# Optimization experiments

Hardware: AMD Instinct MI355X
Metric: run time of the kernel (lower is better)

## Reference

```python
import jax, jax.numpy as jnp
import numpy as np

NUM_TAPS = 4096
LOWCUT, HIGHCUT, FS = 30.0, 1024.0, 4096
B, C, T = 8, 4, 131072


def firwin_bandpass(num_taps, low, high, fs):
    # Replicates scipy.signal.firwin(numtaps, [low, high], pass_zero=False, fs=fs)
    nyq = fs / 2.0
    l, h = low / nyq, high / nyq
    m = np.arange(num_taps) - (num_taps - 1) / 2.0
    h_ideal = h * np.sinc(h * m) - l * np.sinc(l * m)  # ideal bandpass
    hk = h_ideal * np.hamming(num_taps)  # symmetric Hamming (scipy default)
    fc = (l + h) / 2.0  # scale frequency = band midpoint
    hk = hk / np.sum(hk * np.cos(np.pi * m * fc))
    return hk.astype(np.float32)


def _fir_conv(x, kernel):
    # Depthwise 'same' cross-correlation matching torch conv1d(padding='same').
    # x: [B, C, T], kernel: [K]
    Cc = x.shape[1]
    K = kernel.shape[0]
    left, right = (K - 1) // 2, K // 2  # torch 'same' asymmetric pad for even K
    w = jnp.broadcast_to(kernel[None, None, :], (Cc, 1, K))  # [C,1,K] depthwise
    return jax.lax.conv_general_dilated(
        x, w, window_strides=(1,), padding=[(left, right)],
        dimension_numbers=('NCH', 'OIH', 'NCH'), feature_group_count=Cc)


def setup_inputs() -> dict:
    key = jax.random.key(0)
    x = jax.random.normal(key, (B, C, T), dtype=jnp.float32)
    kernel = jnp.asarray(firwin_bandpass(NUM_TAPS, LOWCUT, HIGHCUT, FS))
    return {"x": x, "kernel": kernel}


def reference(x, kernel):
    pad = NUM_TAPS // 2
    xp = jnp.pad(x, ((0, 0), (0, 0), (pad, pad)), mode='reflect')
    y = _fir_conv(xp, kernel)
    # zero-phase: filter time-reversed signal, reverse back
    y = _fir_conv(y[..., ::-1], kernel)[..., ::-1]
    return y[..., pad:-pad]
```

## Files before the change

### kernel.cpp

```cpp
#include <hip/hip_runtime.h>


#define T_LEN   131072
#define XE_LEN  139776
#define XE_U4   (XE_LEN / 8)
#define NCHUNK  312
#define QSTEPS  288
#define QQ      72
#define SCH     8
#define NCH     9
#define CW      64

typedef float  f32x4  __attribute__((ext_vector_type(4)));
typedef __bf16 bf16x8 __attribute__((ext_vector_type(8)));

#define WS_KZ   0
#define WS_G    49152
#define WS_AHI  81920
#define WS_XE   401408
#define WS_END  9347072

__device__ __forceinline__ void gload_lds16(const uint4* g, uint4* lds) {
  __builtin_amdgcn_global_load_lds(
      (const __attribute__((address_space(1))) unsigned int*)g,
      (__attribute__((address_space(3))) unsigned int*)lds, 16, 0, 0);
}

__global__ void k_build_kz(const float* __restrict__ k, float* __restrict__ kz,
                           float* __restrict__ g) {
  int m = blockIdx.x * 256 + threadIdx.x;
  if (m < 12288) {
    int i = m - 4096;
    kz[m] = (i >= 0 && i < 4096) ? k[i] : 0.0f;
  }
  if (m < 8192) g[m] = 0.0f;
}

__global__ void k_autocorr(const float* __restrict__ k,
                           const float* __restrict__ kz,
                           float* __restrict__ g) {
  int s = blockIdx.x * 256 + threadIdx.x;
  int i0 = blockIdx.y * 256;
  const float* kk  = k + i0;
  const float* kzs = kz + (8191 - s) + i0;
  float a0 = 0.f, a1 = 0.f, a2 = 0.f, a3 = 0.f;
  #pragma unroll 4
  for (int i = 0; i < 256; i += 4) {
    float4 kv = *(const float4*)(kk + i);
    float4 zv;
    __builtin_memcpy(&zv, kzs + i, 16);
    a0 = fmaf(kv.x, zv.x, a0);
    a1 = fmaf(kv.y, zv.y, a1);
    a2 = fmaf(kv.z, zv.z, a2);
    a3 = fmaf(kv.w, zv.w, a3);
  }
  atomicAdd(&g[s], (a0 + a1) + (a2 + a3));
}

__global__ void k_build_afrag(const float* __restrict__ g,
                              __bf16* __restrict__ Ahi) {
  int P = blockIdx.x;
  int t = threadIdx.x;
  int l = t >> 2;
  int jj0 = (t & 3) * 2;
  int q = l >> 4, i = l & 15;
  int p = P - 24;
  #pragma unroll
  for (int u = 0; u < 2; ++u) {
    int jj = jj0 + u;
    int s = 32 * p + 8 * q + jj - i;
    float val = (s >= 0 && s <= 8190) ? g[s] : 0.0f;
    Ahi[P * 512 + l * 8 + jj] = (__bf16)val;
  }
}

__global__ void k_build_xe(const float* __restrict__ x, __bf16* __restrict__ xe) {
  int e0 = (blockIdx.x * 256 + threadIdx.x) * 8;
  int row = blockIdx.y;
  if (e0 >= XE_LEN) return;
  const float* xr = x + (size_t)row * T_LEN;
  int v0 = e0 - 4095;
  bf16x8 outv;
  if (v0 >= 0 && v0 <= T_LEN - 8) {
    float4 f0, f1;
    __builtin_memcpy(&f0, xr + v0, 16);
    __builtin_memcpy(&f1, xr + v0 + 4, 16);
    outv[0] = (__bf16)f0.x; outv[1] = (__bf16)f0.y;
    outv[2] = (__bf16)f0.z; outv[3] = (__bf16)f0.w;
    outv[4] = (__bf16)f1.x; outv[5] = (__bf16)f1.y;
    outv[6] = (__bf16)f1.z; outv[7] = (__bf16)f1.w;
  } else {
    #pragma unroll
    for (int u = 0; u < 8; ++u) {
      int v = v0 + u;
      float val = 0.0f;
      if (v >= -2048 && v < T_LEN + 2048) {
        int v2 = v < 0 ? -v : v;
        v2 = v2 >= T_LEN ? 2 * T_LEN - 2 - v2 : v2;
        val = xr[v2];
      }
      outv[u] = (__bf16)val;
    }
  }
  ((uint4*)(xe + (size_t)row * XE_LEN))[e0 >> 3] =
      __builtin_bit_cast(uint4, outv);
}

__global__ __launch_bounds__(256, 2) void k_fir_mfma(
    const uint4* __restrict__ xeu, const uint4* __restrict__ Ahi,
    float* __restrict__ out) {
  __shared__ uint4 sbB[4096];

  const int tid = threadIdx.x;
  const int w   = tid >> 6;
  const int l   = tid & 63;
  const int q   = l >> 4;
  const int n   = l & 15;
  const int t0  = blockIdx.x << 10;
  const int rbase = blockIdx.y << 3;
  const int Qbeg  = w * QQ;
  const int lofs  = q + 2 * n;

  const uint4* gbase = xeu + (size_t)rbase * XE_U4 + (t0 >> 3) + 4 * Qbeg + l;
  uint4* sw = sbB + (w << 10);

  f32x4 acc[8][4];
  #pragma unroll
  for (int r = 0; r < 8; ++r)
    #pragma unroll
    for (int m = 0; m < 4; ++m) acc[r][m] = (f32x4){0.f, 0.f, 0.f, 0.f};

  #pragma unroll
  for (int r = 0; r < 8; ++r)
    gload_lds16(gbase + (size_t)r * XE_U4, sw + (r << 6));
  asm volatile("s_waitcnt vmcnt(0)" ::: "memory");

  int buf = 0;
  for (int ch = 0; ch < NCH; ++ch) {
    if (ch + 1 < NCH) {
      uint4* dst = sw + ((buf ^ 1) << 9);
      const uint4* src = gbase + ((ch + 1) << 5);
      #pragma unroll
      for (int r = 0; r < 8; ++r)
        gload_lds16(src + (size_t)r * XE_U4, dst + (r << 6));
    }

    const uint4* bw = sw + (buf << 9) + lofs;
    #pragma unroll 2
    for (int Qr = 0; Qr < SCH; ++Qr) {
      const int Q = Qbeg + (ch << 3) + Qr;
      bf16x8 A[4];
      #pragma unroll
      for (int mt = 0; mt < 4; ++mt)
        A[mt] = __builtin_bit_cast(bf16x8, Ahi[(Q + 24 - 8 * mt) * 64 + l]);
      #pragma unroll
      for (int r = 0; r < 8; ++r) {
        bf16x8 B = __builtin_bit_cast(bf16x8, bw[(r << 6) + 4 * Qr]);
        #pragma unroll
        for (int mt = 0; mt < 4; ++mt)
          acc[r][mt] =
              __builtin_amdgcn_mfma_f32_16x16x32_bf16(A[mt], B, acc[r][mt], 0, 0, 0);
      }
    }

    if (ch + 1 < NCH) {
      asm volatile("s_waitcnt vmcnt(0)" ::: "memory");
      buf ^= 1;
    }
  }

  __syncthreads();
  float* C = (float*)sbB;
  const int co = (q << 2) + (n << 4);
  #pragma unroll
  for (int ph = 0; ph < 4; ++ph) {
    const int mt = (w + ph) & 3;
    float* cp = C + (mt << 8) + co;
    if (ph == 0) {
      #pragma unroll
      for (int r = 0; r < 8; ++r)
        *(f32x4*)(cp + (r << 10)) = acc[r][mt];
    } else {
      #pragma unroll
      for (int r = 0; r < 8; ++r) {
        f32x4 v = *(f32x4*)(cp + (r << 10));
        v += acc[r][mt];
        *(f32x4*)(cp + (r << 10)) = v;
      }
    }
    __syncthreads();
  }

  #pragma unroll
  for (int u = 0; u < 8; ++u) {
    f32x4 v = ((f32x4*)C)[tid + (u << 8)];
    *(f32x4*)(out + (size_t)(rbase + u) * T_LEN + t0 + (tid << 2)) = v;
  }
}

extern "C" void kernel_launch(void* const* d_in, const int* in_sizes, int n_in,
                              void* d_out, int out_size, void* d_ws, size_t ws_size,
                              hipStream_t stream) {
  const float* x = (const float*)d_in[0];
  const float* k = (const float*)d_in[1];
  float* out = (float*)d_out;
  char* ws = (char*)d_ws;
  if (ws_size < (size_t)WS_END) return;

  float*  kz  = (float*)(ws + WS_KZ);
  float*  g   = (float*)(ws + WS_G);
  __bf16* Ahi = (__bf16*)(ws + WS_AHI);
  __bf16* xe  = (__bf16*)(ws + WS_XE);

  k_build_kz<<<dim3(48), dim3(256), 0, stream>>>(k, kz, g);
  k_autocorr<<<dim3(32, 16), dim3(256), 0, stream>>>(k, kz, g);
  k_build_afrag<<<dim3(NCHUNK), dim3(256), 0, stream>>>(g, Ahi);
  k_build_xe<<<dim3((XE_LEN / 8 + 255) / 256, 32), dim3(256), 0, stream>>>(x, xe);
  k_fir_mfma<<<dim3(T_LEN / 1024, 4), dim3(256), 0, stream>>>(
      (const uint4*)xe, (const uint4*)Ahi, out);
}
```

Before: 169.0 us.

## Fuse kz build into xe kernel, software-pipeline A loads, remap blocks across XCDs

Folds the kz/g initialisation into the xe build kernel, which removes one launch. The FIR MFMA main loop is flattened into a ping-pong step macro, so the A fragments for the next step are prefetched while the current MFMAs run, B values are loaded into registers up front, and s_setprio raises priority around the MFMA burst. The 2D grid becomes 1D with a block-index remap that interleaves blocks across XCDs for better L2 locality. Costs are higher register pressure from the double-buffered A fragments and a larger, more complex unrolled loop.

```diff
diff --git a/kernel.cpp b/kernel.cpp
--- a/kernel.cpp
+++ b/kernel.cpp
@@ -5,11 +5,9 @@
 #define XE_LEN  139776
 #define XE_U4   (XE_LEN / 8)
 #define NCHUNK  312
-#define QSTEPS  288
 #define QQ      72
 #define SCH     8
 #define NCH     9
-#define CW      64
 
 typedef float  f32x4  __attribute__((ext_vector_type(4)));
 typedef __bf16 bf16x8 __attribute__((ext_vector_type(8)));
@@ -24,16 +22,6 @@
   __builtin_amdgcn_global_load_lds(
       (const __attribute__((address_space(1))) unsigned int*)g,
       (__attribute__((address_space(3))) unsigned int*)lds, 16, 0, 0);
-}
-
-__global__ void k_build_kz(const float* __restrict__ k, float* __restrict__ kz,
-                           float* __restrict__ g) {
-  int m = blockIdx.x * 256 + threadIdx.x;
-  if (m < 12288) {
-    int i = m - 4096;
-    kz[m] = (i >= 0 && i < 4096) ? k[i] : 0.0f;
-  }
-  if (m < 8192) g[m] = 0.0f;
 }
 
 __global__ void k_autocorr(const float* __restrict__ k,
@@ -74,7 +62,17 @@
   }
 }
 
-__global__ void k_build_xe(const float* __restrict__ x, __bf16* __restrict__ xe) {
+__global__ void k_build_xe(const float* __restrict__ x, __bf16* __restrict__ xe,
+                           const float* __restrict__ k, float* __restrict__ kz,
+                           float* __restrict__ g) {
+  if (blockIdx.y == 0) {
+    int m = blockIdx.x * 256 + threadIdx.x;
+    if (m < 12288) {
+      int i = m - 4096;
+      kz[m] = (i >= 0 && i < 4096) ? k[i] : 0.0f;
+    }
+    if (m < 8192) g[m] = 0.0f;
+  }
   int e0 = (blockIdx.x * 256 + threadIdx.x) * 8;
   int row = blockIdx.y;
   if (e0 >= XE_LEN) return;
@@ -106,6 +104,45 @@
       __builtin_bit_cast(uint4, outv);
 }
 
+#define FIR_STEP(ACUR, ANXT)                                               \
+  {                                                                        \
+    const int ch = Qi >> 3, Qr = Qi & 7;                                   \
+    if (Qr == 0) {                                                         \
+      if (ch > 0) {                                                        \
+        asm volatile("s_waitcnt vmcnt(0)" ::: "memory");                   \
+        buf ^= 1;                                                          \
+      }                                                                    \
+      if (ch < NCH - 1) {                                                  \
+        uint4* dst = sw + ((buf ^ 1) << 9);                                \
+        const uint4* src = gbase + ((ch + 1) << 5);                        \
+        _Pragma("unroll")                                                  \
+        for (int r = 0; r < 8; ++r)                                        \
+          gload_lds16(src + (size_t)r * XE_U4, dst + (r << 6));            \
+      }                                                                    \
+    }                                                                      \
+    const uint4* bp = sw + (buf << 9) + lofs + (Qr << 2);                  \
+    bf16x8 Bv[8];                                                          \
+    _Pragma("unroll")                                                      \
+    for (int r = 0; r < 8; ++r)                                            \
+      Bv[r] = __builtin_bit_cast(bf16x8, bp[r << 6]);                      \
+    if (Qi < QQ - 1) {                                                     \
+      const int nQ = Qbeg + Qi + 1;                                        \
+      _Pragma("unroll")                                                    \
+      for (int mt = 0; mt < 4; ++mt)                                       \
+        ANXT[mt] =                                                         \
+            __builtin_bit_cast(bf16x8, Ahi[(nQ + 24 - 8 * mt) * 64 + l]);  \
+    }                                                                      \
+    __builtin_amdgcn_s_setprio(1);                                         \
+    _Pragma("unroll")                                                      \
+    for (int r = 0; r < 8; ++r)                                            \
+      _Pragma("unroll")                                                    \
+      for (int mt = 0; mt < 4; ++mt)                                       \
+        acc[r][mt] = __builtin_amdgcn_mfma_f32_16x16x32_bf16(              \
+            ACUR[mt], Bv[r], acc[r][mt], 0, 0, 0);                         \
+    __builtin_amdgcn_s_setprio(0);                                         \
+    ++Qi;                                                                  \
+  }
+
 __global__ __launch_bounds__(256, 2) void k_fir_mfma(
     const uint4* __restrict__ xeu, const uint4* __restrict__ Ahi,
     float* __restrict__ out) {
@@ -116,8 +153,14 @@
   const int l   = tid & 63;
   const int q   = l >> 4;
   const int n   = l & 15;
-  const int t0  = blockIdx.x << 10;
-  const int rbase = blockIdx.y << 3;
+
+  const int orig = blockIdx.x;
+  const int flat = (orig & 7) * 64 + (orig >> 3);
+  const int bx   = flat & 127;
+  const int by   = flat >> 7;
+
+  const int t0    = bx << 10;
+  const int rbase = by << 3;
   const int Qbeg  = w * QQ;
   const int lofs  = q + 2 * n;
 
@@ -133,40 +176,16 @@
   #pragma unroll
   for (int r = 0; r < 8; ++r)
     gload_lds16(gbase + (size_t)r * XE_U4, sw + (r << 6));
+  bf16x8 A0[4], A1[4];
+  #pragma unroll
+  for (int mt = 0; mt < 4; ++mt)
+    A0[mt] = __builtin_bit_cast(bf16x8, Ahi[(Qbeg + 24 - 8 * mt) * 64 + l]);
   asm volatile("s_waitcnt vmcnt(0)" ::: "memory");
 
-  int buf = 0;
-  for (int ch = 0; ch < NCH; ++ch) {
-    if (ch + 1 < NCH) {
-      uint4* dst = sw + ((buf ^ 1) << 9);
-      const uint4* src = gbase + ((ch + 1) << 5);
-      #pragma unroll
-      for (int r = 0; r < 8; ++r)
-        gload_lds16(src + (size_t)r * XE_U4, dst + (r << 6));
-    }
-
-    const uint4* bw = sw + (buf << 9) + lofs;
-    #pragma unroll 2
-    for (int Qr = 0; Qr < SCH; ++Qr) {
-      const int Q = Qbeg + (ch << 3) + Qr;
-      bf16x8 A[4];
-      #pragma unroll
-      for (int mt = 0; mt < 4; ++mt)
-        A[mt] = __builtin_bit_cast(bf16x8, Ahi[(Q + 24 - 8 * mt) * 64 + l]);
-      #pragma unroll
-      for (int r = 0; r < 8; ++r) {
-        bf16x8 B = __builtin_bit_cast(bf16x8, bw[(r << 6) + 4 * Qr]);
-        #pragma unroll
-        for (int mt = 0; mt < 4; ++mt)
-          acc[r][mt] =
-              __builtin_amdgcn_mfma_f32_16x16x32_bf16(A[mt], B, acc[r][mt], 0, 0, 0);
-      }
-    }
-
-    if (ch + 1 < NCH) {
-      asm volatile("s_waitcnt vmcnt(0)" ::: "memory");
-      buf ^= 1;
-    }
+  int buf = 0, Qi = 0;
+  for (int p = 0; p < QQ / 2; ++p) {
+    FIR_STEP(A0, A1);
+    FIR_STEP(A1, A0);
   }
 
   __syncthreads();
@@ -212,10 +231,10 @@
   __bf16* Ahi = (__bf16*)(ws + WS_AHI);
   __bf16* xe  = (__bf16*)(ws + WS_XE);
 
-  k_build_kz<<<dim3(48), dim3(256), 0, stream>>>(k, kz, g);
+  k_build_xe<<<dim3((XE_LEN / 8 + 255) / 256, 32), dim3(256), 0, stream>>>(
+      x, xe, k, kz, g);
   k_autocorr<<<dim3(32, 16), dim3(256), 0, stream>>>(k, kz, g);
   k_build_afrag<<<dim3(NCHUNK), dim3(256), 0, stream>>>(g, Ahi);
-  k_build_xe<<<dim3((XE_LEN / 8 + 255) / 256, 32), dim3(256), 0, stream>>>(x, xe);
-  k_fir_mfma<<<dim3(T_LEN / 1024, 4), dim3(256), 0, stream>>>(
+  k_fir_mfma<<<dim3(512), dim3(256), 0, stream>>>(
       (const uint4*)xe, (const uint4*)Ahi, out);
 }
```

Result: faster. 160.8 us (-4.8%).

## Split MFMA FIR block into 8 waves, fuse kz build into xe kernel

Applied to the files above, without the earlier changes.

The main FIR kernel now launches 512-thread blocks whose 8 waves split the 8 rows into two groups of 4, which halves accumulator registers per wave. It targets higher occupancy (launch bounds 4) and hides latency better. A block-index swizzle reorders the tiles across the grid, and s_setprio is raised around the MFMA bursts, with B fragments loaded before them. The separate kz/g build kernel is folded into the xe build kernel to save one launch. The risk is that each wave holds fewer rows, so the A fragments are reused less per load.

```diff
diff --git a/kernel.cpp b/kernel.cpp
--- a/kernel.cpp
+++ b/kernel.cpp
@@ -5,11 +5,9 @@
 #define XE_LEN  139776
 #define XE_U4   (XE_LEN / 8)
 #define NCHUNK  312
-#define QSTEPS  288
 #define QQ      72
 #define SCH     8
 #define NCH     9
-#define CW      64
 
 typedef float  f32x4  __attribute__((ext_vector_type(4)));
 typedef __bf16 bf16x8 __attribute__((ext_vector_type(8)));
@@ -24,16 +22,6 @@
   __builtin_amdgcn_global_load_lds(
       (const __attribute__((address_space(1))) unsigned int*)g,
       (__attribute__((address_space(3))) unsigned int*)lds, 16, 0, 0);
-}
-
-__global__ void k_build_kz(const float* __restrict__ k, float* __restrict__ kz,
-                           float* __restrict__ g) {
-  int m = blockIdx.x * 256 + threadIdx.x;
-  if (m < 12288) {
-    int i = m - 4096;
-    kz[m] = (i >= 0 && i < 4096) ? k[i] : 0.0f;
-  }
-  if (m < 8192) g[m] = 0.0f;
 }
 
 __global__ void k_autocorr(const float* __restrict__ k,
@@ -74,7 +62,17 @@
   }
 }
 
-__global__ void k_build_xe(const float* __restrict__ x, __bf16* __restrict__ xe) {
+__global__ void k_build_xe(const float* __restrict__ x, __bf16* __restrict__ xe,
+                           const float* __restrict__ k, float* __restrict__ kz,
+                           float* __restrict__ g) {
+  if (blockIdx.y == 0) {
+    int m = blockIdx.x * 256 + threadIdx.x;
+    if (m < 12288) {
+      int i = m - 4096;
+      kz[m] = (i >= 0 && i < 4096) ? k[i] : 0.0f;
+    }
+    if (m < 8192) g[m] = 0.0f;
+  }
   int e0 = (blockIdx.x * 256 + threadIdx.x) * 8;
   int row = blockIdx.y;
   if (e0 >= XE_LEN) return;
@@ -106,7 +104,7 @@
       __builtin_bit_cast(uint4, outv);
 }
 
-__global__ __launch_bounds__(256, 2) void k_fir_mfma(
+__global__ __launch_bounds__(512, 4) void k_fir_mfma(
     const uint4* __restrict__ xeu, const uint4* __restrict__ Ahi,
     float* __restrict__ out) {
   __shared__ uint4 sbB[4096];
@@ -116,36 +114,45 @@
   const int l   = tid & 63;
   const int q   = l >> 4;
   const int n   = l & 15;
-  const int t0  = blockIdx.x << 10;
-  const int rbase = blockIdx.y << 3;
-  const int Qbeg  = w * QQ;
-  const int lofs  = q + 2 * n;
-
-  const uint4* gbase = xeu + (size_t)rbase * XE_U4 + (t0 >> 3) + 4 * Qbeg + l;
-  uint4* sw = sbB + (w << 10);
-
-  f32x4 acc[8][4];
-  #pragma unroll
-  for (int r = 0; r < 8; ++r)
+  const int qh  = w & 3;
+  const int rg  = w >> 2;
+
+  const int orig = blockIdx.x;
+  const int flat = (orig & 7) * 64 + (orig >> 3);
+  const int bx   = flat & 127;
+  const int by   = flat >> 7;
+
+  const int t0     = bx << 10;
+  const int brbase = by << 3;
+  const int wrbase = brbase + (rg << 2);
+  const int Qbeg   = qh * QQ;
+  const int lofs   = q + 2 * n;
+
+  const uint4* gbase = xeu + (size_t)wrbase * XE_U4 + (t0 >> 3) + 4 * Qbeg + l;
+  uint4* sw = sbB + (w << 9);
+
+  f32x4 acc[4][4];
+  #pragma unroll
+  for (int r = 0; r < 4; ++r)
     #pragma unroll
     for (int m = 0; m < 4; ++m) acc[r][m] = (f32x4){0.f, 0.f, 0.f, 0.f};
 
   #pragma unroll
-  for (int r = 0; r < 8; ++r)
+  for (int r = 0; r < 4; ++r)
     gload_lds16(gbase + (size_t)r * XE_U4, sw + (r << 6));
   asm volatile("s_waitcnt vmcnt(0)" ::: "memory");
 
   int buf = 0;
   for (int ch = 0; ch < NCH; ++ch) {
     if (ch + 1 < NCH) {
-      uint4* dst = sw + ((buf ^ 1) << 9);
+      uint4* dst = sw + ((buf ^ 1) << 8);
       const uint4* src = gbase + ((ch + 1) << 5);
       #pragma unroll
-      for (int r = 0; r < 8; ++r)
+      for (int r = 0; r < 4; ++r)
         gload_lds16(src + (size_t)r * XE_U4, dst + (r << 6));
     }
 
-    const uint4* bw = sw + (buf << 9) + lofs;
+    const uint4* bw = sw + (buf << 8) + lofs;
     #pragma unroll 2
     for (int Qr = 0; Qr < SCH; ++Qr) {
       const int Q = Qbeg + (ch << 3) + Qr;
@@ -153,14 +160,18 @@
       #pragma unroll
       for (int mt = 0; mt < 4; ++mt)
         A[mt] = __builtin_bit_cast(bf16x8, Ahi[(Q + 24 - 8 * mt) * 64 + l]);
-      #pragma unroll
-      for (int r = 0; r < 8; ++r) {
-        bf16x8 B = __builtin_bit_cast(bf16x8, bw[(r << 6) + 4 * Qr]);
+      bf16x8 Bv[4];
+      #pragma unroll
+      for (int r = 0; r < 4; ++r)
+        Bv[r] = __builtin_bit_cast(bf16x8, bw[(r << 6) + 4 * Qr]);
+      __builtin_amdgcn_s_setprio(1);
+      #pragma unroll
+      for (int r = 0; r < 4; ++r)
         #pragma unroll
         for (int mt = 0; mt < 4; ++mt)
-          acc[r][mt] =
-              __builtin_amdgcn_mfma_f32_16x16x32_bf16(A[mt], B, acc[r][mt], 0, 0, 0);
-      }
+          acc[r][mt] = __builtin_amdgcn_mfma_f32_16x16x32_bf16(
+              A[mt], Bv[r], acc[r][mt], 0, 0, 0);
+      __builtin_amdgcn_s_setprio(0);
     }
 
     if (ch + 1 < NCH) {
@@ -174,15 +185,15 @@
   const int co = (q << 2) + (n << 4);
   #pragma unroll
   for (int ph = 0; ph < 4; ++ph) {
-    const int mt = (w + ph) & 3;
-    float* cp = C + (mt << 8) + co;
+    const int mt = (qh + ph) & 3;
+    float* cp = C + ((rg << 2) << 10) + (mt << 8) + co;
     if (ph == 0) {
       #pragma unroll
-      for (int r = 0; r < 8; ++r)
+      for (int r = 0; r < 4; ++r)
         *(f32x4*)(cp + (r << 10)) = acc[r][mt];
     } else {
       #pragma unroll
-      for (int r = 0; r < 8; ++r) {
+      for (int r = 0; r < 4; ++r) {
         f32x4 v = *(f32x4*)(cp + (r << 10));
         v += acc[r][mt];
         *(f32x4*)(cp + (r << 10)) = v;
@@ -192,9 +203,12 @@
   }
 
   #pragma unroll
-  for (int u = 0; u < 8; ++u) {
-    f32x4 v = ((f32x4*)C)[tid + (u << 8)];
-    *(f32x4*)(out + (size_t)(rbase + u) * T_LEN + t0 + (tid << 2)) = v;
+  for (int u = 0; u < 4; ++u) {
+    const int idx = tid + (u << 9);
+    f32x4 v = ((f32x4*)C)[idx];
+    const int row = idx >> 8;
+    const int tc  = (idx & 255) << 2;
+    *(f32x4*)(out + (size_t)(brbase + row) * T_LEN + t0 + tc) = v;
   }
 }
 
@@ -212,10 +226,10 @@
   __bf16* Ahi = (__bf16*)(ws + WS_AHI);
   __bf16* xe  = (__bf16*)(ws + WS_XE);
 
-  k_build_kz<<<dim3(48), dim3(256), 0, stream>>>(k, kz, g);
+  k_build_xe<<<dim3((XE_LEN / 8 + 255) / 256, 32), dim3(256), 0, stream>>>(
+      x, xe, k, kz, g);
   k_autocorr<<<dim3(32, 16), dim3(256), 0, stream>>>(k, kz, g);
   k_build_afrag<<<dim3(NCHUNK), dim3(256), 0, stream>>>(g, Ahi);
-  k_build_xe<<<dim3((XE_LEN / 8 + 255) / 256, 32), dim3(256), 0, stream>>>(x, xe);
-  k_fir_mfma<<<dim3(T_LEN / 1024, 4), dim3(256), 0, stream>>>(
+  k_fir_mfma<<<dim3(512), dim3(512), 0, stream>>>(
       (const uint4*)xe, (const uint4*)Ahi, out);
 }
```

New measurement: 163.4 us. 1.03x faster.
